# Optimization experiments

Measured on AMD Instinct MI355X. Metric: run time of the kernel, lower is better.

## Reference

```python
import jax, jax.numpy as jnp
import numpy as np

N, D_IM, D_CLI = 2048, 1024, 64
EPS = 1e-12  # F.normalize eps


def setup_inputs() -> dict:
    key = jax.random.key(0)
    k1, k2, k3, k4 = jax.random.split(key, 4)
    phi_im = jax.random.normal(k1, (N, D_IM), dtype=jnp.float32)
    phi_cli = jax.random.normal(k2, (N, D_CLI), dtype=jnp.float32)
    t = jax.random.randint(k3, (N, 2), 0, 3, dtype=jnp.int64)
    traumatic = jax.random.randint(k4, (N,), 0, 2, dtype=jnp.int64)
    return {"phi_im": phi_im, "phi_cli": phi_cli, "t": t, "traumatic": traumatic}


def _l2norm(x):
    n = jnp.sqrt(jnp.sum(x * x, axis=1, keepdims=True))
    return x / jnp.maximum(n, EPS)


def _pair_block(S, ma, mb):
    # S: [N,N] full cosine similarity; ma, mb: [N] bool group masks.
    valid = ma[:, None] & mb[None, :]
    mat = jnp.where(valid, S, 0.0)            # scatter-into-zero matrix semantics
    masked = jnp.where(valid, S, jnp.inf)     # masked argmin = nearest (least similar) pair
    flat = jnp.argmin(masked.reshape(-1))
    i = flat // S.shape[1]
    j = flat % S.shape[1]
    return mat, masked.reshape(-1)[flat], jnp.stack([i, j])


def reference(phi_im, phi_cli, t, traumatic):
    im_n = _l2norm(phi_im)
    cli_n = _l2norm(phi_cli)
    # single batched GEMM replaces the per-pair python loops
    S_im = im_n @ im_n.T    # [N,N]
    S_cli = cli_n @ cli_n.T  # [N,N]

    t1 = t[:, 1]
    m0 = (t1 == 0) & (traumatic == 1)
    m1 = t1 == 1
    m2 = t1 == 2

    mats, vals, idxs = [], [], []
    for S in (S_im, S_cli):
        for (ma, mb) in ((m0, m1), (m0, m2), (m1, m2)):
            mat, v, ij = _pair_block(S, ma, mb)
            mats.append(mat)
            vals.append(v)
            idxs.append(ij)
    sims = jnp.stack(mats)           # [6, N, N]: im_01, im_02, im_12, cli_01, cli_02, cli_12
    min_vals = jnp.stack(vals)       # [6]
    min_idx = jnp.stack(idxs)        # [6, 2]
    return sims, min_vals, min_idx
```

## Files before the change

### kernel.cpp

```cpp
#include <hip/hip_runtime.h>
#include <stdint.h>

#define NROW 2048
#define D_IM 1024
#define D_CLI 64
#define EPSF 1e-12f
#define NN ((size_t)NROW * (size_t)NROW)
#define GRID_GEMM 800

typedef __attribute__((ext_vector_type(8))) short bf16x8;
typedef __attribute__((ext_vector_type(4))) float f32x4;

#define OFF_PACKED   0
#define OFF_CNT      64
#define OFF_CAT      128
#define OFF_LISTS    8320
#define OFF_POS      32896
#define OFF_COLINFO  41216
#define OFF_INVIM    65792
#define OFF_INVCLI   73984
#define OFF_PIM      82176
#define OFF_PCLI     8470784
#define OFF_SC       8995072

__device__ __forceinline__ unsigned int enc_f32(float x) {
    unsigned int u = __float_as_uint(x);
    return (u & 0x80000000u) ? ~u : (u | 0x80000000u);
}
__device__ __forceinline__ unsigned short bf16rn(float x) {
    unsigned int u = __float_as_uint(x);
    return (unsigned short)((u + 0x7FFFu + ((u >> 16) & 1u)) >> 16);
}
__device__ __forceinline__ float bf16tof(unsigned short h) {
    return __uint_as_float(((unsigned int)h) << 16);
}

__global__ __launch_bounds__(256)
void prepscan_kernel(const float* __restrict__ phi_im,
                     const float* __restrict__ phi_cli,
                     const int* __restrict__ t,
                     const int* __restrict__ traumatic,
                     float* __restrict__ inv_im,
                     float* __restrict__ inv_cli,
                     char* __restrict__ pim,
                     char* __restrict__ pcli,
                     int* __restrict__ cnt,
                     int* __restrict__ catArr,
                     int* __restrict__ lists,
                     int* __restrict__ posIn,
                     unsigned int* __restrict__ colinfo,
                     unsigned long long* __restrict__ packed) {
    __shared__ unsigned long long shmem[256];
    const int tid = threadIdx.x;

    if (blockIdx.x == NROW) {
        int cats[8];
        unsigned long long mycnt = 0;
        #pragma unroll
        for (int e = 0; e < 8; e++) {
            int r = tid * 8 + e;
            int t1 = t[2 * r + 1];
            int tr = traumatic[r];
            int c = (t1 == 1) ? 1 : ((t1 == 2) ? 2 : ((tr == 1) ? 0 : 3));
            cats[e] = c;
            catArr[r] = c;
            if (c < 3) mycnt += 1ULL << (21 * c);
        }
        shmem[tid] = mycnt;
        __syncthreads();
        for (int off = 1; off < 256; off <<= 1) {
            unsigned long long v = (tid >= off) ? shmem[tid - off] : 0ULL;
            __syncthreads();
            shmem[tid] += v;
            __syncthreads();
        }
        unsigned long long excl = shmem[tid] - mycnt;
        unsigned long long tot = shmem[255];
        unsigned int loc[3];
        #pragma unroll
        for (int c = 0; c < 3; c++)
            loc[c] = (unsigned int)(excl >> (21 * c)) & 0x1FFFFFu;
        #pragma unroll
        for (int e = 0; e < 8; e++) {
            int r = tid * 8 + e;
            int c = cats[e];
            unsigned int slot = 0xFFFFFFFFu;
            if (c < 3) {
                slot = loc[c]++;
                lists[c * 2048 + slot] = r;
                posIn[r] = (int)slot;
            }
            colinfo[0 * 2048 + r] = (c == 1) ? slot : 0xFFFFFFFFu;
            colinfo[1 * 2048 + r] = (c == 2) ? slot : 0xFFFFFFFFu;
            colinfo[2 * 2048 + r] = (c == 2) ? slot : 0xFFFFFFFFu;
        }
        if (tid == 0) {
            cnt[0] = (int)(tot & 0x1FFFFFu);
            cnt[1] = (int)((tot >> 21) & 0x1FFFFFu);
            cnt[2] = (int)((tot >> 42) & 0x1FFFFFu);
            cnt[3] = 0;
        }
        if (tid < 6) packed[tid] = 0xFFFFFFFFFFFFFFFFULL;
        return;
    }

    float* sred = (float*)shmem;
    const int r = blockIdx.x;

    float4 v = ((const float4*)(phi_im + (size_t)r * D_IM))[tid];
    float a[4] = {v.x, v.y, v.z, v.w};
    unsigned short h4[4], l4[4];
    #pragma unroll
    for (int e = 0; e < 4; e++) {
        h4[e] = bf16rn(a[e]);
        l4[e] = bf16rn(a[e] - bf16tof(h4[e]));
    }
    {
        char* rowb = pim + (size_t)r * 4096 + (tid >> 1) * 32 + (tid & 1) * 8;
        *(ushort4*)rowb = make_ushort4(h4[0], h4[1], h4[2], h4[3]);
        *(ushort4*)(rowb + 16) = make_ushort4(l4[0], l4[1], l4[2], l4[3]);
    }
    sred[tid] = a[0] * a[0] + a[1] * a[1] + a[2] * a[2] + a[3] * a[3];
    __syncthreads();
    for (int off = 128; off > 0; off >>= 1) {
        if (tid < off) sred[tid] += sred[tid + off];
        __syncthreads();
    }
    if (tid == 0) inv_im[r] = 1.0f / fmaxf(sqrtf(sred[0]), EPSF);

    if (tid < 16) {
        float4 c = ((const float4*)(phi_cli + (size_t)r * D_CLI))[tid];
        float b[4] = {c.x, c.y, c.z, c.w};
        unsigned short ch[4], cl[4];
        #pragma unroll
        for (int e = 0; e < 4; e++) {
            ch[e] = bf16rn(b[e]);
            cl[e] = bf16rn(b[e] - bf16tof(ch[e]));
        }
        char* rowb = pcli + (size_t)r * 256 + (tid >> 1) * 32 + (tid & 1) * 8;
        *(ushort4*)rowb = make_ushort4(ch[0], ch[1], ch[2], ch[3]);
        *(ushort4*)(rowb + 16) = make_ushort4(cl[0], cl[1], cl[2], cl[3]);
    }
    if (tid < 64) {
        float c = phi_cli[(size_t)r * D_CLI + tid];
        float cs = c * c;
        #pragma unroll
        for (int off = 32; off > 0; off >>= 1) cs += __shfl_down(cs, off, 64);
        if (tid == 0) inv_cli[r] = 1.0f / fmaxf(sqrtf(cs), EPSF);
    }
}

#define LOAD_SET(s, AH, AL, BH, BL)                                        \
    {                                                                      \
        const int kb_ = (s) * 128;                                         \
        _Pragma("unroll") for (int mt = 0; mt < 4; mt++) {                 \
            AH[mt] = *(const bf16x8*)(pX + offA[mt] + kb_);                \
            AL[mt] = *(const bf16x8*)(pX + offA[mt] + kb_ + 16);           \
            BH[mt] = *(const bf16x8*)(pX + offB[mt] + kb_);                \
            BL[mt] = *(const bf16x8*)(pX + offB[mt] + kb_ + 16);           \
        }                                                                  \
    }
#define MFMA_SET(AH, AL, BH, BL)                                           \
    _Pragma("unroll") for (int mt = 0; mt < 4; mt++)                       \
        _Pragma("unroll") for (int nt = 0; nt < 4; nt++) {                 \
            acc[mt][nt] = __builtin_amdgcn_mfma_f32_16x16x32_bf16(         \
                AH[mt], BH[nt], acc[mt][nt], 0, 0, 0);                     \
            acc[mt][nt] = __builtin_amdgcn_mfma_f32_16x16x32_bf16(         \
                AH[mt], BL[nt], acc[mt][nt], 0, 0, 0);                     \
            acc[mt][nt] = __builtin_amdgcn_mfma_f32_16x16x32_bf16(         \
                AL[mt], BH[nt], acc[mt][nt], 0, 0, 0);                     \
        }

__global__ __launch_bounds__(64, 2)
void gemm_kernel(const char* __restrict__ pim,
                 const char* __restrict__ pcli,
                 const float* __restrict__ inv_im,
                 const float* __restrict__ inv_cli,
                 const int* __restrict__ cnt,
                 const int* __restrict__ lists,
                 const int* __restrict__ catArr,
                 unsigned short* __restrict__ Sc,
                 float* __restrict__ out,
                 unsigned long long* __restrict__ packed) {
    if (blockIdx.x >= GRID_GEMM) {
        const int b = blockIdx.x - GRID_GEMM;
        const int pz = b >> 11;
        const int row = b & 2047;
        const int p = pz - 3 * (pz / 3);
        const int rowcat = (p == 2) ? 1 : 0;
        if (catArr[row] == rowcat) return;
        float* orow = out + (size_t)pz * NN + (size_t)row * NROW;
        const int lane = threadIdx.x;
        const f32x4 z4 = (f32x4){0.f, 0.f, 0.f, 0.f};
        #pragma unroll
        for (int s = 0; s < 8; s++)
            __builtin_nontemporal_store(z4, (f32x4*)orow + lane + s * 64);
        return;
    }

    __shared__ float sIA[64], sIB[64];
    __shared__ int sRA[64], sRB[64];

    const int n0 = cnt[0], n1 = cnt[1], n2 = cnt[2];
    const int tA = (n0 + 63) >> 6, tB = (n1 + 63) >> 6, tC = (n2 + 63) >> 6;
    const int T0 = tA * tB, T1 = tA * tC, T2 = tB * tC;
    const int tot = T0 + T1 + T2;
    int bid = blockIdx.x;
    if (bid >= 2 * tot) return;
    int z = 0;
    if (bid >= tot) { z = 1; bid -= tot; }
    const size_t s0 = (size_t)(tA << 6) * (tB << 6);
    const size_t s1 = (size_t)(tA << 6) * (tC << 6);
    const size_t s2 = (size_t)(tB << 6) * (tC << 6);
    size_t scoff = z ? (s0 + s1 + s2) : 0;
    int gx, nA, nB, nBpad, pp;
    const int *lA, *lB;
    if (bid < T0)           { pp = 0; gx = tB; nA = n0; nB = n1; lA = lists;        lB = lists + 2048; nBpad = tB << 6; }
    else if (bid < T0 + T1) { bid -= T0;      scoff += s0;      pp = 1; gx = tC; nA = n0; nB = n2; lA = lists;        lB = lists + 4096; nBpad = tC << 6; }
    else                    { bid -= T0 + T1; scoff += s0 + s1; pp = 2; gx = tC; nA = n1; nB = n2; lA = lists + 2048; lB = lists + 4096; nBpad = tC << 6; }
    const int by = bid / gx, bx = bid % gx;
    const int i0 = by << 6, j0 = bx << 6;
    const int pz = z * 3 + pp;

    const char* __restrict__ pX = z ? pcli : pim;
    const float* __restrict__ inv = z ? inv_cli : inv_im;
    const int steps = z ? (D_CLI / 32) : (D_IM / 32);
    const size_t stride = z ? 256 : 4096;
    const int lane = threadIdx.x;

    {
        int ia = lA[min(i0 + lane, nA - 1)];
        int ib = lB[min(j0 + lane, nB - 1)];
        sRA[lane] = ia; sRB[lane] = ib;
        sIA[lane] = inv[ia]; sIB[lane] = inv[ib];
    }
    __syncthreads();

    const int mrow = lane & 15;
    const int quad = lane >> 4;
    size_t offA[4], offB[4];
    #pragma unroll
    for (int mt = 0; mt < 4; mt++) {
        offA[mt] = (size_t)sRA[mt * 16 + mrow] * stride + quad * 32;
        offB[mt] = (size_t)sRB[mt * 16 + mrow] * stride + quad * 32;
    }

    f32x4 acc[4][4];
    #pragma unroll
    for (int mt = 0; mt < 4; mt++)
        #pragma unroll
        for (int nt = 0; nt < 4; nt++)
            acc[mt][nt] = (f32x4){0.f, 0.f, 0.f, 0.f};

    bf16x8 A0h[4], A0l[4], B0h[4], B0l[4];
    bf16x8 A1h[4], A1l[4], B1h[4], B1l[4];
    LOAD_SET(0, A0h, A0l, B0h, B0l);
    for (int s = 0; s < steps; s += 2) {
        if (s + 1 < steps) LOAD_SET(s + 1, A1h, A1l, B1h, B1l);
        MFMA_SET(A0h, A0l, B0h, B0l);
        if (s + 2 < steps) LOAD_SET(s + 2, A0h, A0l, B0h, B0l);
        if (s + 1 < steps) MFMA_SET(A1h, A1l, B1h, B1l);
    }

    unsigned long long best = 0xFFFFFFFFFFFFFFFFULL;
    #pragma unroll
    for (int mt = 0; mt < 4; mt++)
        #pragma unroll
        for (int nt = 0; nt < 4; nt++) {
            const int cloc = nt * 16 + mrow;
            const float ivb = sIB[cloc];
            const unsigned int jcol = (unsigned int)sRB[cloc];
            #pragma unroll
            for (int rr = 0; rr < 4; rr++) {
                const int rloc = mt * 16 + quad * 4 + rr;
                float sv = acc[mt][nt][rr] * (sIA[rloc] * ivb);
                Sc[scoff + (size_t)(i0 + rloc) * nBpad + (j0 + cloc)] = bf16rn(sv);
                unsigned long long pk =
                    ((unsigned long long)enc_f32(sv) << 32) |
                    ((unsigned int)sRA[rloc] * (unsigned int)NROW + jcol);
                if (pk < best) best = pk;
            }
        }
    #pragma unroll
    for (int off = 32; off > 0; off >>= 1) {
        unsigned long long o = __shfl_down(best, off, 64);
        if (o < best) best = o;
    }
    if (lane == 0) atomicMin(&packed[pz], best);
}

__global__ __launch_bounds__(256)
void writer_kernel(const unsigned short* __restrict__ Sc,
                   const int* __restrict__ cnt,
                   const int* __restrict__ catArr,
                   const int* __restrict__ posIn,
                   const unsigned int* __restrict__ colinfo,
                   float* __restrict__ out,
                   const unsigned long long* __restrict__ packed) {
    const int b = blockIdx.x;
    const int tid = threadIdx.x;
    if (b == 6 * NROW) {
        const int p = tid;
        if (p < 6) {
            unsigned long long pk = packed[p];
            float v;
            unsigned int flat;
            if (pk == 0xFFFFFFFFFFFFFFFFULL) { v = __builtin_huge_valf(); flat = 0u; }
            else {
                unsigned int key = (unsigned int)(pk >> 32);
                flat = (unsigned int)pk;
                unsigned int bits = (key & 0x80000000u) ? (key ^ 0x80000000u) : ~key;
                v = __uint_as_float(bits);
            }
            out[6 * NN + p] = v;
            out[6 * NN + 6 + 2 * p + 0] = (float)(flat >> 11);
            out[6 * NN + 6 + 2 * p + 1] = (float)(flat & 2047u);
        }
        return;
    }
    const int pz = b >> 11;
    const int row = b & 2047;
    const int z = pz / 3, p = pz - 3 * z;

    const int rowcat = (p == 2) ? 1 : 0;
    if (catArr[row] != rowcat) return;

    float* orow = out + (size_t)pz * NN + (size_t)row * NROW;

    const int n0 = cnt[0], n1 = cnt[1], n2 = cnt[2];
    const int tA = (n0 + 63) >> 6, tB = (n1 + 63) >> 6, tC = (n2 + 63) >> 6;
    const size_t s0 = (size_t)(tA << 6) * (tB << 6);
    const size_t s1 = (size_t)(tA << 6) * (tC << 6);
    const size_t s2 = (size_t)(tB << 6) * (tC << 6);
    size_t scoff = z ? (s0 + s1 + s2) : 0;
    int nBpad;
    if (p == 0)      { nBpad = tB << 6; }
    else if (p == 1) { scoff += s0;      nBpad = tC << 6; }
    else             { scoff += s0 + s1; nBpad = tC << 6; }

    const unsigned short* srow = Sc + scoff + (size_t)posIn[row] * nBpad;
    const uint4* cinfo4 = (const uint4*)(colinfo + p * 2048);

    #pragma unroll
    for (int seg = 0; seg < 2; seg++) {
        const int j4 = tid + seg * 256;
        uint4 inf = cinfo4[j4];
        f32x4 vv;
        vv[0] = (inf.x != 0xFFFFFFFFu) ? bf16tof(srow[inf.x]) : 0.f;
        vv[1] = (inf.y != 0xFFFFFFFFu) ? bf16tof(srow[inf.y]) : 0.f;
        vv[2] = (inf.z != 0xFFFFFFFFu) ? bf16tof(srow[inf.z]) : 0.f;
        vv[3] = (inf.w != 0xFFFFFFFFu) ? bf16tof(srow[inf.w]) : 0.f;
        __builtin_nontemporal_store(vv, (f32x4*)orow + j4);
    }
}

extern "C" void kernel_launch(void* const* d_in, const int* in_sizes, int n_in,
                              void* d_out, int out_size, void* d_ws, size_t ws_size,
                              hipStream_t stream) {
    const float* phi_im = (const float*)d_in[0];
    const float* phi_cli = (const float*)d_in[1];
    const int* t = (const int*)d_in[2];
    const int* traumatic = (const int*)d_in[3];
    float* out = (float*)d_out;

    char* ws = (char*)d_ws;
    unsigned long long* packed = (unsigned long long*)(ws + OFF_PACKED);
    int* cnt = (int*)(ws + OFF_CNT);
    int* catArr = (int*)(ws + OFF_CAT);
    int* lists = (int*)(ws + OFF_LISTS);
    int* posIn = (int*)(ws + OFF_POS);
    unsigned int* colinfo = (unsigned int*)(ws + OFF_COLINFO);
    float* inv_im = (float*)(ws + OFF_INVIM);
    float* inv_cli = (float*)(ws + OFF_INVCLI);
    char* pim = ws + OFF_PIM;
    char* pcli = ws + OFF_PCLI;
    unsigned short* Sc = (unsigned short*)(ws + OFF_SC);

    prepscan_kernel<<<NROW + 1, 256, 0, stream>>>(
        phi_im, phi_cli, t, traumatic, inv_im, inv_cli, pim, pcli,
        cnt, catArr, lists, posIn, colinfo, packed);
    gemm_kernel<<<GRID_GEMM + 6 * NROW, 64, 0, stream>>>(
        pim, pcli, inv_im, inv_cli, cnt, lists, catArr, Sc, out, packed);
    writer_kernel<<<6 * NROW + 1, 256, 0, stream>>>(Sc, cnt, catArr, posIn,
                                                    colinfo, out, packed);
}
```

Baseline: 163.4 us.

## Split GEMM K-loop across four waves and spread zero-fill over all kernels

The GEMM block grows from one wave to four. Each wave computes a quarter of the K steps, and the partial accumulators are reduced through shared memory, with each wave finishing one 16-column slice. The zero-filling of rows outside the masked groups is now spread out: prepscan fills pz=0, the gemm tail fills pz=1..3, and the writer fills pz=4..5. The aim is more latency hiding per tile and zero-fill that overlaps with other work. The cost is a large LDS buffer for the partial sums (about 48KB), which may lower occupancy, plus an extra synchronisation.

```diff
diff --git a/kernel.cpp b/kernel.cpp
--- a/kernel.cpp
+++ b/kernel.cpp
@@ -49,9 +49,22 @@
                      int* __restrict__ lists,
                      int* __restrict__ posIn,
                      unsigned int* __restrict__ colinfo,
-                     unsigned long long* __restrict__ packed) {
+                     unsigned long long* __restrict__ packed,
+                     float* __restrict__ out) {
     __shared__ unsigned long long shmem[256];
     const int tid = threadIdx.x;
+
+    if (blockIdx.x > NROW) {
+        const int row = blockIdx.x - (NROW + 1);
+        const int t1 = t[2 * row + 1];
+        const int tr = traumatic[row];
+        if (t1 == 0 && tr == 1) return;
+        float* orow = out + (size_t)row * NROW;
+        const f32x4 z4 = (f32x4){0.f, 0.f, 0.f, 0.f};
+        __builtin_nontemporal_store(z4, (f32x4*)orow + tid);
+        __builtin_nontemporal_store(z4, (f32x4*)orow + tid + 256);
+        return;
+    }
 
     if (blockIdx.x == NROW) {
         int cats[8];
@@ -171,7 +184,7 @@
                 AL[mt], BH[nt], acc[mt][nt], 0, 0, 0);                     \
         }
 
-__global__ __launch_bounds__(64, 2)
+__global__ __launch_bounds__(256, 2)
 void gemm_kernel(const char* __restrict__ pim,
                  const char* __restrict__ pcli,
                  const float* __restrict__ inv_im,
@@ -182,24 +195,25 @@
                  unsigned short* __restrict__ Sc,
                  float* __restrict__ out,
                  unsigned long long* __restrict__ packed) {
+    const int tid = threadIdx.x;
+
     if (blockIdx.x >= GRID_GEMM) {
         const int b = blockIdx.x - GRID_GEMM;
-        const int pz = b >> 11;
+        const int pzf = 1 + (b >> 11);
         const int row = b & 2047;
-        const int p = pz - 3 * (pz / 3);
+        const int p = (pzf < 3) ? pzf : pzf - 3;
         const int rowcat = (p == 2) ? 1 : 0;
         if (catArr[row] == rowcat) return;
-        float* orow = out + (size_t)pz * NN + (size_t)row * NROW;
-        const int lane = threadIdx.x;
+        float* orow = out + (size_t)pzf * NN + (size_t)row * NROW;
         const f32x4 z4 = (f32x4){0.f, 0.f, 0.f, 0.f};
-        #pragma unroll
-        for (int s = 0; s < 8; s++)
-            __builtin_nontemporal_store(z4, (f32x4*)orow + lane + s * 64);
+        __builtin_nontemporal_store(z4, (f32x4*)orow + tid);
+        __builtin_nontemporal_store(z4, (f32x4*)orow + tid + 256);
         return;
     }
 
     __shared__ float sIA[64], sIB[64];
     __shared__ int sRA[64], sRB[64];
+    __shared__ f32x4 sAcc[4][4][3][64];
 
     const int n0 = cnt[0], n1 = cnt[1], n2 = cnt[2];
     const int tA = (n0 + 63) >> 6, tB = (n1 + 63) >> 6, tC = (n2 + 63) >> 6;
@@ -226,13 +240,14 @@
     const float* __restrict__ inv = z ? inv_cli : inv_im;
     const int steps = z ? (D_CLI / 32) : (D_IM / 32);
     const size_t stride = z ? 256 : 4096;
-    const int lane = threadIdx.x;
-
-    {
-        int ia = lA[min(i0 + lane, nA - 1)];
-        int ib = lB[min(j0 + lane, nB - 1)];
-        sRA[lane] = ia; sRB[lane] = ib;
-        sIA[lane] = inv[ia]; sIB[lane] = inv[ib];
+    const int lane = tid & 63;
+    const int wid = tid >> 6;
+
+    if (tid < 64) {
+        int ia = lA[min(i0 + tid, nA - 1)];
+        int ib = lB[min(j0 + tid, nB - 1)];
+        sRA[tid] = ia; sRB[tid] = ib;
+        sIA[tid] = inv[ia]; sIB[tid] = inv[ib];
     }
     __syncthreads();
 
@@ -252,35 +267,50 @@
         for (int nt = 0; nt < 4; nt++)
             acc[mt][nt] = (f32x4){0.f, 0.f, 0.f, 0.f};
 
+    const int spw = (steps + 3) >> 2;
+    const int sBeg = wid * spw;
+    const int sEnd = min(steps, sBeg + spw);
+
     bf16x8 A0h[4], A0l[4], B0h[4], B0l[4];
     bf16x8 A1h[4], A1l[4], B1h[4], B1l[4];
-    LOAD_SET(0, A0h, A0l, B0h, B0l);
-    for (int s = 0; s < steps; s += 2) {
-        if (s + 1 < steps) LOAD_SET(s + 1, A1h, A1l, B1h, B1l);
-        MFMA_SET(A0h, A0l, B0h, B0l);
-        if (s + 2 < steps) LOAD_SET(s + 2, A0h, A0l, B0h, B0l);
-        if (s + 1 < steps) MFMA_SET(A1h, A1l, B1h, B1l);
-    }
+    if (sBeg < sEnd) {
+        LOAD_SET(sBeg, A0h, A0l, B0h, B0l);
+        for (int s = sBeg; s < sEnd; s += 2) {
+            if (s + 1 < sEnd) LOAD_SET(s + 1, A1h, A1l, B1h, B1l);
+            MFMA_SET(A0h, A0l, B0h, B0l);
+            if (s + 2 < sEnd) LOAD_SET(s + 2, A0h, A0l, B0h, B0l);
+            if (s + 1 < sEnd) MFMA_SET(A1h, A1l, B1h, B1l);
+        }
+    }
+
+    #pragma unroll
+    for (int mt = 0; mt < 4; mt++)
+        #pragma unroll
+        for (int nt = 0; nt < 4; nt++)
+            if (nt != wid) sAcc[wid][mt][nt - (nt > wid ? 1 : 0)][lane] = acc[mt][nt];
+    __syncthreads();
 
     unsigned long long best = 0xFFFFFFFFFFFFFFFFULL;
-    #pragma unroll
-    for (int mt = 0; mt < 4; mt++)
-        #pragma unroll
-        for (int nt = 0; nt < 4; nt++) {
-            const int cloc = nt * 16 + mrow;
-            const float ivb = sIB[cloc];
-            const unsigned int jcol = (unsigned int)sRB[cloc];
-            #pragma unroll
-            for (int rr = 0; rr < 4; rr++) {
-                const int rloc = mt * 16 + quad * 4 + rr;
-                float sv = acc[mt][nt][rr] * (sIA[rloc] * ivb);
-                Sc[scoff + (size_t)(i0 + rloc) * nBpad + (j0 + cloc)] = bf16rn(sv);
-                unsigned long long pk =
-                    ((unsigned long long)enc_f32(sv) << 32) |
-                    ((unsigned int)sRA[rloc] * (unsigned int)NROW + jcol);
-                if (pk < best) best = pk;
-            }
-        }
+    const int cloc = wid * 16 + mrow;
+    const float ivb = sIB[cloc];
+    const unsigned int jcol = (unsigned int)sRB[cloc];
+    #pragma unroll
+    for (int mt = 0; mt < 4; mt++) {
+        f32x4 facc = acc[mt][wid];
+        #pragma unroll
+        for (int w2 = 0; w2 < 4; w2++)
+            if (w2 != wid) facc += sAcc[w2][mt][wid - (wid > w2 ? 1 : 0)][lane];
+        #pragma unroll
+        for (int rr = 0; rr < 4; rr++) {
+            const int rloc = mt * 16 + quad * 4 + rr;
+            float sv = facc[rr] * (sIA[rloc] * ivb);
+            Sc[scoff + (size_t)(i0 + rloc) * nBpad + (j0 + cloc)] = bf16rn(sv);
+            unsigned long long pk =
+                ((unsigned long long)enc_f32(sv) << 32) |
+                ((unsigned int)sRA[rloc] * (unsigned int)NROW + jcol);
+            if (pk < best) best = pk;
+        }
+    }
     #pragma unroll
     for (int off = 32; off > 0; off >>= 1) {
         unsigned long long o = __shfl_down(best, off, 64);
@@ -323,7 +353,14 @@
     const int z = pz / 3, p = pz - 3 * z;
 
     const int rowcat = (p == 2) ? 1 : 0;
-    if (catArr[row] != rowcat) return;
+    if (catArr[row] != rowcat) {
+        if (pz < 4) return;
+        float* orow = out + (size_t)pz * NN + (size_t)row * NROW;
+        const f32x4 z4 = (f32x4){0.f, 0.f, 0.f, 0.f};
+        __builtin_nontemporal_store(z4, (f32x4*)orow + tid);
+        __builtin_nontemporal_store(z4, (f32x4*)orow + tid + 256);
+        return;
+    }
 
     float* orow = out + (size_t)pz * NN + (size_t)row * NROW;
 
@@ -376,10 +413,10 @@
     char* pcli = ws + OFF_PCLI;
     unsigned short* Sc = (unsigned short*)(ws + OFF_SC);
 
-    prepscan_kernel<<<NROW + 1, 256, 0, stream>>>(
+    prepscan_kernel<<<2 * NROW + 1, 256, 0, stream>>>(
         phi_im, phi_cli, t, traumatic, inv_im, inv_cli, pim, pcli,
-        cnt, catArr, lists, posIn, colinfo, packed);
-    gemm_kernel<<<GRID_GEMM + 6 * NROW, 64, 0, stream>>>(
+        cnt, catArr, lists, posIn, colinfo, packed, out);
+    gemm_kernel<<<GRID_GEMM + 3 * NROW, 256, 0, stream>>>(
         pim, pcli, inv_im, inv_cli, cnt, lists, catArr, Sc, out, packed);
     writer_kernel<<<6 * NROW + 1, 256, 0, stream>>>(Sc, cnt, catArr, posIn,
                                                     colinfo, out, packed);
```

Measured after the change: 179.3 us. 1.1x slower.
